# Kernel tuning notes

Measured on AMD Instinct MI355X. Metric: run time of the kernel, lower is better.

Reference implementation:

```python
import jax, jax.numpy as jnp
import numpy as np

EMBED_DIM = 768
NUM_HEADS = 12
HEAD_DIM = EMBED_DIM // NUM_HEADS  # 64
SCALE = HEAD_DIM ** -0.5
B, S = 32, 512


def setup_inputs() -> dict:
    key = jax.random.key(0)
    ks = jax.random.split(key, 10)
    std = EMBED_DIM ** -0.5
    hidden_states = jax.random.normal(ks[0], (B, S, EMBED_DIM), dtype=jnp.float32)
    # causal mask: 0 on/below diagonal, large negative above
    neg = jnp.full((S, S), -1e9, dtype=jnp.float32)
    causal_attention_mask = jnp.broadcast_to(
        jnp.triu(neg, k=1)[None, None, :, :], (B, 1, S, S)
    ).astype(jnp.float32)
    Wq = jax.random.normal(ks[1], (EMBED_DIM, EMBED_DIM), dtype=jnp.float32) * std
    bq = jnp.zeros((EMBED_DIM,), dtype=jnp.float32)
    Wk = jax.random.normal(ks[2], (EMBED_DIM, EMBED_DIM), dtype=jnp.float32) * std
    bk = jnp.zeros((EMBED_DIM,), dtype=jnp.float32)
    Wv = jax.random.normal(ks[3], (EMBED_DIM, EMBED_DIM), dtype=jnp.float32) * std
    bv = jnp.zeros((EMBED_DIM,), dtype=jnp.float32)
    Wo = jax.random.normal(ks[4], (EMBED_DIM, EMBED_DIM), dtype=jnp.float32) * std
    bo = jnp.zeros((EMBED_DIM,), dtype=jnp.float32)
    return {
        "hidden_states": hidden_states,
        "causal_attention_mask": causal_attention_mask,
        "Wq": Wq, "bq": bq, "Wk": Wk, "bk": bk,
        "Wv": Wv, "bv": bv, "Wo": Wo, "bo": bo,
    }


def reference(hidden_states, causal_attention_mask, Wq, bq, Wk, bk, Wv, bv, Wo, bo):
    b, s, e = hidden_states.shape
    # projections; query scaled as in original
    q = (hidden_states @ Wq + bq) * SCALE          # [b,s,e]
    k = hidden_states @ Wk + bk
    v = hidden_states @ Wv + bv
    # [b,h,s,d]
    q = q.reshape(b, s, NUM_HEADS, HEAD_DIM).transpose(0, 2, 1, 3)
    k = k.reshape(b, s, NUM_HEADS, HEAD_DIM).transpose(0, 2, 1, 3)
    v = v.reshape(b, s, NUM_HEADS, HEAD_DIM).transpose(0, 2, 1, 3)
    scores = jnp.einsum("bhqd,bhkd->bhqk", q, k) + causal_attention_mask
    attn = jax.nn.softmax(scores, axis=-1)
    out = jnp.einsum("bhqk,bhkd->bhqd", attn, v)   # [b,h,s,d]
    out = out.transpose(0, 2, 1, 3).reshape(b, s, e)
    return out @ Wo + bo
```

## Files before the change

### kernel.cpp

```cpp
#include <hip/hip_runtime.h>
#include <hip/hip_bf16.h>

typedef __attribute__((ext_vector_type(8))) short bf16x8;
typedef __attribute__((ext_vector_type(4))) float f32x4;
typedef unsigned short u16;
typedef unsigned int u32;

#define MFMA16(a,b,c) __builtin_amdgcn_mfma_f32_16x16x32_bf16((a),(b),(c),0,0,0)
#define FENCE() asm volatile("" ::: "memory")
#define BARRIER() do { FENCE(); __builtin_amdgcn_s_barrier(); FENCE(); } while (0)
#define WAITV(N) asm volatile("s_waitcnt vmcnt(" #N ")" ::: "memory")

__device__ __forceinline__ u16 f2bf(float f) {
  union { float f; u32 u; } c; c.f = f;
  u32 u = c.u;
  return (u16)((u + 0x7FFFu + ((u >> 16) & 1u)) >> 16);
}

__device__ __forceinline__ u32 pk2(float lo, float hi) {
  __hip_bfloat162 h2 = __float22bfloat162_rn(float2{lo, hi});
  union { __hip_bfloat162 h; u32 u; } c; c.h = h2; return c.u;
}

__device__ __forceinline__ void gl_lds16(const u16* g, u16* l) {
  __builtin_amdgcn_global_load_lds((const __attribute__((address_space(1))) void*)g,
                                   (__attribute__((address_space(3))) void*)l, 16, 0, 0);
}

__global__ __launch_bounds__(256) void prep(const float* __restrict__ X,
                                            u16* __restrict__ Xb,
                                            const float* __restrict__ Wq,
                                            const float* __restrict__ Wk,
                                            const float* __restrict__ Wv,
                                            const float* __restrict__ Wo,
                                            u16* __restrict__ WT) {
  const int blk = blockIdx.x, tid = threadIdx.x;
  if (blk < 6144) {
    int i = (blk * 256 + tid) * 8;
    const float4* p = (const float4*)(X + i);
    float4 a = p[0], b = p[1];
    union { u16 h[8]; uint4 v; } o;
    o.h[0] = f2bf(a.x); o.h[1] = f2bf(a.y); o.h[2] = f2bf(a.z); o.h[3] = f2bf(a.w);
    o.h[4] = f2bf(b.x); o.h[5] = f2bf(b.y); o.h[6] = f2bf(b.z); o.h[7] = f2bf(b.w);
    *(uint4*)(Xb + i) = o.v;
  } else {
    __shared__ float t[32][33];
    const int q = blk - 6144;
    const int w = q / 576, p = q % 576;
    const float* W = (w == 0) ? Wq : (w == 1) ? Wk : (w == 2) ? Wv : Wo;
    u16* D = WT + (size_t)w * 768 * 768;
    const int n0 = (p % 24) * 32, k0 = (p / 24) * 32;
    const int tx = tid & 31, ty = tid >> 5;
#pragma unroll
    for (int i = 0; i < 4; ++i)
      t[ty + i * 8][tx] = W[(size_t)(k0 + ty + i * 8) * 768 + n0 + tx];
    __syncthreads();
#pragma unroll
    for (int i = 0; i < 4; ++i)
      D[(size_t)(n0 + ty + i * 8) * 768 + k0 + tx] = f2bf(t[tx][ty + i * 8]);
  }
}


#define STA2(bu, t, q) do { \
    const int r_ = (q) * 64 + (tid >> 3); \
    const int g_ = tid & 7; \
    gl_lds16(A + (size_t)(M0 + r_) * 768 + (t) * 64 + ((g_ ^ (r_ & 7)) << 3), \
             &As[bu][r_ * 64 + g_ * 8]); \
  } while (0)
#define STB3(bu, t, h) do { \
    const int r_ = (h) * 64 + (tid >> 3); \
    const int g_ = tid & 7; \
    gl_lds16(BT + (size_t)(N0 + r_) * 768 + (t) * 64 + ((g_ ^ (r_ & 7)) << 3), \
             &Bs[bu][r_ * 64 + g_ * 8]); \
  } while (0)

template <int MODE>
__global__ __launch_bounds__(512, 4)
void gemmR(const u16* __restrict__ A, const u16* __restrict__ BT,
           const float* __restrict__ b0, const float* __restrict__ b1,
           const float* __restrict__ b2,
           u16* __restrict__ oQ, u16* __restrict__ oK, u16* __restrict__ oV,
           float* __restrict__ oF, int nN) {
  constexpr int NT = 12;
  __shared__ __align__(16) u16 As[2][128 * 64];
  __shared__ __align__(16) u16 Bs[2][192 * 64];
  const int tid = threadIdx.x;
  const int wave = tid >> 6, lane = tid & 63;
  const int lg = lane >> 4, l15 = lane & 15;
  const int wr = wave >> 2, wc = wave & 3;
  const int bi = blockIdx.x;
  const int j = bi >> 3;
  const int M0 = ((bi & 7) * 16 + j / nN) * 128;
  const int N0 = (j % nN) * 192;

  f32x4 acc[4][3] = {};

  STA2(0, 0, 0); STA2(0, 0, 1);
  STB3(0, 0, 0); STB3(0, 0, 1); STB3(0, 0, 2);

#pragma unroll
  for (int t = 0; t < NT; ++t) {
    WAITV(0);
    BARRIER();
    if (t + 1 < NT) {
      const int nb = (t + 1) & 1;
      STA2(nb, t + 1, 0); STA2(nb, t + 1, 1);
      STB3(nb, t + 1, 0); STB3(nb, t + 1, 1); STB3(nb, t + 1, 2);
    }
    const int bb = t & 1;
    __builtin_amdgcn_s_setprio(1);
    bf16x8 bfr[3][2];
#pragma unroll
    for (int nt = 0; nt < 3; ++nt)
#pragma unroll
      for (int kh = 0; kh < 2; ++kh) {
        const int row = wc * 48 + nt * 16 + l15;
        bfr[nt][kh] = *(const bf16x8*)&Bs[bb][row * 64 + (((kh * 4 + lg) ^ (row & 7)) << 3)];
      }
#pragma unroll
    for (int mt = 0; mt < 4; ++mt) {
      bf16x8 af[2];
#pragma unroll
      for (int kh = 0; kh < 2; ++kh) {
        const int row = wr * 64 + mt * 16 + l15;
        af[kh] = *(const bf16x8*)&As[bb][row * 64 + (((kh * 4 + lg) ^ (row & 7)) << 3)];
      }
#pragma unroll
      for (int nt = 0; nt < 3; ++nt)
#pragma unroll
        for (int kh = 0; kh < 2; ++kh)
          acc[mt][nt] = MFMA16(af[kh], bfr[nt][kh], acc[mt][nt]);
    }
    __builtin_amdgcn_s_setprio(0);
  }

#pragma unroll
  for (int mt = 0; mt < 4; ++mt) {
    const int r0 = M0 + wr * 64 + mt * 16 + lg * 4;
#pragma unroll
    for (int nt = 0; nt < 3; ++nt) {
      const int ng = N0 + wc * 48 + nt * 16 + l15;
      f32x4 v = acc[mt][nt];
      if (MODE == 1) {
        const float bb = b0[ng];
#pragma unroll
        for (int r = 0; r < 4; ++r)
          oF[(size_t)(r0 + r) * 768 + ng] = v[r] + bb;
      } else {
        const int mat = ng / 768;
        const int col = ng - mat * 768;
        const float bb = (mat == 0 ? b0 : (mat == 1 ? b1 : b2))[col];
        if (mat == 0) {
#pragma unroll
          for (int r = 0; r < 4; ++r)
            oQ[(size_t)(r0 + r) * 768 + col] = f2bf((v[r] + bb) * 0.125f);
        } else if (mat == 1) {
#pragma unroll
          for (int r = 0; r < 4; ++r)
            oK[(size_t)(r0 + r) * 768 + col] = f2bf(v[r] + bb);
        } else {
          const int hh = col >> 6, dd = col & 63;
#pragma unroll
          for (int r = 0; r < 4; ++r) {
            const int rr = r0 + r;
            const int bbx = rr >> 9, ss = rr & 511;
            oV[((size_t)(bbx * 12 + hh) * 64 + dd) * 512 + ss] = f2bf(v[r] + bb);
          }
        }
      }
    }
  }
}

#define STG(bu, kt) do { \
    gl_lds16(Kg0 + (size_t)((kt) * 64 + srow) * 768 + sgr * 8, \
             &Ks[bu][srow * 64 + (tid & 7) * 8]); \
    gl_lds16(Vg0 + (size_t)srow * 512 + (kt) * 64 + sgr * 8, \
             &Vs[bu][srow * 64 + (tid & 7) * 8]); \
  } while (0)

__global__ __launch_bounds__(512)
void flash(const u16* __restrict__ Q, const u16* __restrict__ K,
           const u16* __restrict__ V, u16* __restrict__ O) {
  __shared__ __align__(16) u16 Ks[2][4096];
  __shared__ __align__(16) u16 Vs[2][4096];
  __shared__ __align__(16) u32 Ps[8][16 * 36];
  const int id = blockIdx.x;
  const int qt = id / 384, hb = id % 384;
  const int h = hb % 12, b = hb / 12;
  const int tid = threadIdx.x, wave = tid >> 6, lane = tid & 63;
  const int lg = lane >> 4, l15 = lane & 15;
  const int NT = 2 * qt + 2;
  const int srow = tid >> 3, sgr = (tid & 7) ^ (srow & 7);
  const int qbase = qt * 128 + wave * 16;

  bf16x8 qf[2];
  {
    const u16* qp = Q + (size_t)(b * 512 + qbase + l15) * 768 + h * 64 + lg * 8;
    qf[0] = *(const bf16x8*)qp;
    qf[1] = *(const bf16x8*)(qp + 32);
  }
  f32x4 oacc[4] = {};
  float m_run = -1e30f, l_run = 0.f;
  const u16* Kg0 = K + (size_t)(b * 512) * 768 + h * 64;
  const u16* Vg0 = V + (size_t)(b * 12 + h) * 64 * 512;
  u32* pw = Ps[wave];

  STG(0, 0);
  for (int kt = 0; kt < NT; ++kt) {
    WAITV(0);
    BARRIER();
    if (kt + 1 < NT) STG((kt + 1) & 1, kt + 1);
    const int bu = kt & 1;
    if (kt * 64 <= qbase + 15) {
      f32x4 sc[4] = {};
#pragma unroll
      for (int kc = 0; kc < 2; ++kc)
#pragma unroll
        for (int t = 0; t < 4; ++t) {
          const int row = t * 16 + l15;
          bf16x8 kf = *(const bf16x8*)&Ks[bu][row * 64 + (((kc * 4 + lg) ^ (l15 & 7)) << 3)];
          sc[t] = MFMA16(kf, qf[kc], sc[t]);
        }
      if (kt * 64 + 63 > qbase) {
#pragma unroll
        for (int t = 0; t < 4; ++t)
#pragma unroll
          for (int r = 0; r < 4; ++r)
            if (kt * 64 + t * 16 + lg * 4 + r > qbase + l15) sc[t][r] = -1e30f;
      }
      float pm = sc[0][0];
#pragma unroll
      for (int t = 0; t < 4; ++t)
#pragma unroll
        for (int r = 0; r < 4; ++r) pm = fmaxf(pm, sc[t][r]);
      pm = fmaxf(pm, __shfl_xor(pm, 16));
      pm = fmaxf(pm, __shfl_xor(pm, 32));
      if (__any(pm > m_run + 8.f)) {
        const float mn = fmaxf(m_run, pm);
        const float fs = __expf(m_run - mn);
        m_run = mn;
        l_run *= fs;
#pragma unroll
        for (int t = 0; t < 4; ++t)
#pragma unroll
          for (int r = 0; r < 4; ++r) oacc[t][r] *= fs;
      }
      float rs = 0.f;
#pragma unroll
      for (int t = 0; t < 4; ++t) {
        float p0 = __expf(sc[t][0] - m_run), p1 = __expf(sc[t][1] - m_run);
        float p2 = __expf(sc[t][2] - m_run), p3 = __expf(sc[t][3] - m_run);
        rs += (p0 + p1) + (p2 + p3);
        pw[l15 * 36 + t * 8 + lg * 2 + 0] = pk2(p0, p1);
        pw[l15 * 36 + t * 8 + lg * 2 + 1] = pk2(p2, p3);
      }
      rs += __shfl_xor(rs, 16);
      rs += __shfl_xor(rs, 32);
      l_run += rs;
#pragma unroll
      for (int kc = 0; kc < 2; ++kc) {
        bf16x8 pf = *(const bf16x8*)&pw[l15 * 36 + kc * 16 + lg * 4];
#pragma unroll
        for (int t = 0; t < 4; ++t) {
          const int row = t * 16 + l15;
          bf16x8 vf = *(const bf16x8*)&Vs[bu][row * 64 + (((kc * 4 + lg) ^ (l15 & 7)) << 3)];
          oacc[t] = MFMA16(vf, pf, oacc[t]);
        }
      }
    }
  }
  const float inv = 1.f / l_run;
  u16* op = O + (size_t)(b * 512 + qbase + l15) * 768 + h * 64;
#pragma unroll
  for (int t = 0; t < 4; ++t) {
    uint2 w;
    w.x = pk2(oacc[t][0] * inv, oacc[t][1] * inv);
    w.y = pk2(oacc[t][2] * inv, oacc[t][3] * inv);
    *(uint2*)(op + t * 16 + lg * 4) = w;
  }
}

extern "C" void kernel_launch(void* const* d_in, const int* in_sizes, int n_in,
                              void* d_out, int out_size, void* d_ws, size_t ws_size,
                              hipStream_t stream) {
  (void)in_sizes; (void)n_in; (void)out_size; (void)ws_size;
  const float* X  = (const float*)d_in[0];
  const float* Wq = (const float*)d_in[2];
  const float* bq = (const float*)d_in[3];
  const float* Wk = (const float*)d_in[4];
  const float* bk = (const float*)d_in[5];
  const float* Wv = (const float*)d_in[6];
  const float* bv = (const float*)d_in[7];
  const float* Wo = (const float*)d_in[8];
  const float* bo = (const float*)d_in[9];
  float* out = (float*)d_out;

  const size_t NME = (size_t)16384 * 768;
  u16* Xb  = (u16*)d_ws;
  u16* Qs  = Xb + NME;
  u16* Kb  = Qs + NME;
  u16* Vt  = Kb + NME;
  u16* WT  = Vt + NME;
  u16* WoT = WT + (size_t)2304 * 768;
  u16* Ao  = Xb;

  prep<<<8448, 256, 0, stream>>>(X, Xb, Wq, Wk, Wv, Wo, WT);
  gemmR<0><<<1536, 512, 0, stream>>>(Xb, WT, bq, bk, bv, Qs, Kb, Vt, nullptr, 12);
  flash<<<1536, 512, 0, stream>>>(Qs, Kb, Vt, Ao);
  gemmR<1><<<512, 512, 0, stream>>>(Ao, WoT, bo, nullptr, nullptr,
                                    nullptr, nullptr, nullptr, out, 4);
}
```

Baseline: 152.3 us.

## Pair causal query tiles per block to balance work and share K/V loads

```diff
diff --git a/kernel.cpp b/kernel.cpp
--- a/kernel.cpp
+++ b/kernel.cpp
@@ -180,29 +180,98 @@
              &Vs[bu][srow * 64 + (tid & 7) * 8]); \
   } while (0)
 
-__global__ __launch_bounds__(512)
+__device__ __forceinline__ void attn_step(const u16* ks, const u16* vs, u32* pw,
+                                          const bf16x8 qf[2], f32x4 oacc[4],
+                                          float& m_run, float& l_run,
+                                          int kt, int qbase, int lg, int l15) {
+  if (kt * 64 > qbase + 15) return;
+  f32x4 sc[4] = {};
+#pragma unroll
+  for (int kc = 0; kc < 2; ++kc)
+#pragma unroll
+    for (int t = 0; t < 4; ++t) {
+      const int row = t * 16 + l15;
+      bf16x8 kf = *(const bf16x8*)&ks[row * 64 + (((kc * 4 + lg) ^ (l15 & 7)) << 3)];
+      sc[t] = MFMA16(kf, qf[kc], sc[t]);
+    }
+  if (kt * 64 + 63 > qbase) {
+#pragma unroll
+    for (int t = 0; t < 4; ++t)
+#pragma unroll
+      for (int r = 0; r < 4; ++r)
+        if (kt * 64 + t * 16 + lg * 4 + r > qbase + l15) sc[t][r] = -1e30f;
+  }
+  float pm = sc[0][0];
+#pragma unroll
+  for (int t = 0; t < 4; ++t)
+#pragma unroll
+    for (int r = 0; r < 4; ++r) pm = fmaxf(pm, sc[t][r]);
+  pm = fmaxf(pm, __shfl_xor(pm, 16));
+  pm = fmaxf(pm, __shfl_xor(pm, 32));
+  if (__any(pm > m_run + 8.f)) {
+    const float mn = fmaxf(m_run, pm);
+    const float fs = __expf(m_run - mn);
+    m_run = mn;
+    l_run *= fs;
+#pragma unroll
+    for (int t = 0; t < 4; ++t)
+#pragma unroll
+      for (int r = 0; r < 4; ++r) oacc[t][r] *= fs;
+  }
+  float rs = 0.f;
+#pragma unroll
+  for (int t = 0; t < 4; ++t) {
+    float p0 = __expf(sc[t][0] - m_run), p1 = __expf(sc[t][1] - m_run);
+    float p2 = __expf(sc[t][2] - m_run), p3 = __expf(sc[t][3] - m_run);
+    rs += (p0 + p1) + (p2 + p3);
+    pw[l15 * 36 + t * 8 + lg * 2 + 0] = pk2(p0, p1);
+    pw[l15 * 36 + t * 8 + lg * 2 + 1] = pk2(p2, p3);
+  }
+  rs += __shfl_xor(rs, 16);
+  rs += __shfl_xor(rs, 32);
+  l_run += rs;
+#pragma unroll
+  for (int kc = 0; kc < 2; ++kc) {
+    bf16x8 pf = *(const bf16x8*)&pw[l15 * 36 + kc * 16 + lg * 4];
+#pragma unroll
+    for (int t = 0; t < 4; ++t) {
+      const int row = t * 16 + l15;
+      bf16x8 vf = *(const bf16x8*)&vs[row * 64 + (((kc * 4 + lg) ^ (l15 & 7)) << 3)];
+      oacc[t] = MFMA16(vf, pf, oacc[t]);
+    }
+  }
+}
+
+__global__ __launch_bounds__(512, 2)
 void flash(const u16* __restrict__ Q, const u16* __restrict__ K,
            const u16* __restrict__ V, u16* __restrict__ O) {
   __shared__ __align__(16) u16 Ks[2][4096];
   __shared__ __align__(16) u16 Vs[2][4096];
   __shared__ __align__(16) u32 Ps[8][16 * 36];
   const int id = blockIdx.x;
-  const int qt = id / 384, hb = id % 384;
+  const int pair = id >> 9 >= 0 ? (id >= 384) : 0;
+  const int hb = id - (pair ? 384 : 0);
   const int h = hb % 12, b = hb / 12;
   const int tid = threadIdx.x, wave = tid >> 6, lane = tid & 63;
   const int lg = lane >> 4, l15 = lane & 15;
-  const int NT = 2 * qt + 2;
+  const int qA = pair ? 2 : 3;
+  const int qB = pair ? 1 : 0;
+  const int NT = 2 * qA + 2;
   const int srow = tid >> 3, sgr = (tid & 7) ^ (srow & 7);
-  const int qbase = qt * 128 + wave * 16;
-
-  bf16x8 qf[2];
+  const int qbaseA = qA * 128 + wave * 16;
+  const int qbaseB = qB * 128 + wave * 16;
+
+  bf16x8 qfA[2], qfB[2];
   {
-    const u16* qp = Q + (size_t)(b * 512 + qbase + l15) * 768 + h * 64 + lg * 8;
-    qf[0] = *(const bf16x8*)qp;
-    qf[1] = *(const bf16x8*)(qp + 32);
-  }
-  f32x4 oacc[4] = {};
-  float m_run = -1e30f, l_run = 0.f;
+    const u16* qp = Q + (size_t)(b * 512 + qbaseA + l15) * 768 + h * 64 + lg * 8;
+    qfA[0] = *(const bf16x8*)qp;
+    qfA[1] = *(const bf16x8*)(qp + 32);
+    const u16* qp2 = Q + (size_t)(b * 512 + qbaseB + l15) * 768 + h * 64 + lg * 8;
+    qfB[0] = *(const bf16x8*)qp2;
+    qfB[1] = *(const bf16x8*)(qp2 + 32);
+  }
+  f32x4 oaccA[4] = {}, oaccB[4] = {};
+  float mA = -1e30f, lA = 0.f, mB = -1e30f, lB = 0.f;
   const u16* Kg0 = K + (size_t)(b * 512) * 768 + h * 64;
   const u16* Vg0 = V + (size_t)(b * 12 + h) * 64 * 512;
   u32* pw = Ps[wave];
@@ -213,72 +282,30 @@
     BARRIER();
     if (kt + 1 < NT) STG((kt + 1) & 1, kt + 1);
     const int bu = kt & 1;
-    if (kt * 64 <= qbase + 15) {
-      f32x4 sc[4] = {};
-#pragma unroll
-      for (int kc = 0; kc < 2; ++kc)
-#pragma unroll
-        for (int t = 0; t < 4; ++t) {
-          const int row = t * 16 + l15;
-          bf16x8 kf = *(const bf16x8*)&Ks[bu][row * 64 + (((kc * 4 + lg) ^ (l15 & 7)) << 3)];
-          sc[t] = MFMA16(kf, qf[kc], sc[t]);
-        }
-      if (kt * 64 + 63 > qbase) {
-#pragma unroll
-        for (int t = 0; t < 4; ++t)
-#pragma unroll
-          for (int r = 0; r < 4; ++r)
-            if (kt * 64 + t * 16 + lg * 4 + r > qbase + l15) sc[t][r] = -1e30f;
-      }
-      float pm = sc[0][0];
-#pragma unroll
-      for (int t = 0; t < 4; ++t)
-#pragma unroll
-        for (int r = 0; r < 4; ++r) pm = fmaxf(pm, sc[t][r]);
-      pm = fmaxf(pm, __shfl_xor(pm, 16));
-      pm = fmaxf(pm, __shfl_xor(pm, 32));
-      if (__any(pm > m_run + 8.f)) {
-        const float mn = fmaxf(m_run, pm);
-        const float fs = __expf(m_run - mn);
-        m_run = mn;
-        l_run *= fs;
-#pragma unroll
-        for (int t = 0; t < 4; ++t)
-#pragma unroll
-          for (int r = 0; r < 4; ++r) oacc[t][r] *= fs;
-      }
-      float rs = 0.f;
-#pragma unroll
-      for (int t = 0; t < 4; ++t) {
-        float p0 = __expf(sc[t][0] - m_run), p1 = __expf(sc[t][1] - m_run);
-        float p2 = __expf(sc[t][2] - m_run), p3 = __expf(sc[t][3] - m_run);
-        rs += (p0 + p1) + (p2 + p3);
-        pw[l15 * 36 + t * 8 + lg * 2 + 0] = pk2(p0, p1);
-        pw[l15 * 36 + t * 8 + lg * 2 + 1] = pk2(p2, p3);
-      }
-      rs += __shfl_xor(rs, 16);
-      rs += __shfl_xor(rs, 32);
-      l_run += rs;
-#pragma unroll
-      for (int kc = 0; kc < 2; ++kc) {
-        bf16x8 pf = *(const bf16x8*)&pw[l15 * 36 + kc * 16 + lg * 4];
-#pragma unroll
-        for (int t = 0; t < 4; ++t) {
-          const int row = t * 16 + l15;
-          bf16x8 vf = *(const bf16x8*)&Vs[bu][row * 64 + (((kc * 4 + lg) ^ (l15 & 7)) << 3)];
-          oacc[t] = MFMA16(vf, pf, oacc[t]);
-        }
-      }
-    }
-  }
-  const float inv = 1.f / l_run;
-  u16* op = O + (size_t)(b * 512 + qbase + l15) * 768 + h * 64;
-#pragma unroll
-  for (int t = 0; t < 4; ++t) {
-    uint2 w;
-    w.x = pk2(oacc[t][0] * inv, oacc[t][1] * inv);
-    w.y = pk2(oacc[t][2] * inv, oacc[t][3] * inv);
-    *(uint2*)(op + t * 16 + lg * 4) = w;
+    attn_step(Ks[bu], Vs[bu], pw, qfA, oaccA, mA, lA, kt, qbaseA, lg, l15);
+    attn_step(Ks[bu], Vs[bu], pw, qfB, oaccB, mB, lB, kt, qbaseB, lg, l15);
+  }
+  {
+    const float inv = 1.f / lA;
+    u16* op = O + (size_t)(b * 512 + qbaseA + l15) * 768 + h * 64;
+#pragma unroll
+    for (int t = 0; t < 4; ++t) {
+      uint2 w;
+      w.x = pk2(oaccA[t][0] * inv, oaccA[t][1] * inv);
+      w.y = pk2(oaccA[t][2] * inv, oaccA[t][3] * inv);
+      *(uint2*)(op + t * 16 + lg * 4) = w;
+    }
+  }
+  {
+    const float inv = 1.f / lB;
+    u16* op = O + (size_t)(b * 512 + qbaseB + l15) * 768 + h * 64;
+#pragma unroll
+    for (int t = 0; t < 4; ++t) {
+      uint2 w;
+      w.x = pk2(oaccB[t][0] * inv, oaccB[t][1] * inv);
+      w.y = pk2(oaccB[t][2] * inv, oaccB[t][3] * inv);
+      *(uint2*)(op + t * 16 + lg * 4) = w;
+    }
   }
 }
 
@@ -308,7 +335,7 @@
 
   prep<<<8448, 256, 0, stream>>>(X, Xb, Wq, Wk, Wv, Wo, WT);
   gemmR<0><<<1536, 512, 0, stream>>>(Xb, WT, bq, bk, bv, Qs, Kb, Vt, nullptr, 12);
-  flash<<<1536, 512, 0, stream>>>(Qs, Kb, Vt, Ao);
+  flash<<<768, 512, 0, stream>>>(Qs, Kb, Vt, Ao);
   gemmR<1><<<512, 512, 0, stream>>>(Ao, WoT, bo, nullptr, nullptr,
                                     nullptr, nullptr, nullptr, out, 4);
 }
```

After: 152.6 us. About the same (+0.1%).
